# Optimization experiments

Hardware: AMD Instinct MI355X
Metric: run time of the kernel (lower is better)

Reference implementation:

```python
import jax, jax.numpy as jnp
import numpy as np

NUM_CAPSULE = 10
DIM_CAPSULE = 16
ROUTINGS = 3
EPS = 1e-7  # K.epsilon()


def squash(x, axis=-1):
    sq_norm = jnp.sum(jnp.square(x), axis=axis, keepdims=True) + EPS
    coeff = jnp.sqrt(sq_norm) / (1.0 + sq_norm)
    return coeff * x


def setup_inputs() -> dict:
    key = jax.random.key(0)
    k1, k2 = jax.random.split(key)
    B, I, Din = 64, 4096, 128
    u_vecs = jax.random.normal(k1, (B, I, Din), dtype=jnp.float32)
    # glorot-ish scale for the capsule kernel (flattened conv1d kernel of size 1)
    W = jax.random.normal(k2, (Din, NUM_CAPSULE * DIM_CAPSULE), dtype=jnp.float32) * 0.06
    return {"u_vecs": u_vecs, "W": W}


def reference(u_vecs, W):
    B, I, Din = u_vecs.shape
    N, D = NUM_CAPSULE, DIM_CAPSULE
    # conv1d with kernel size 1 == per-position matmul
    u_hat = jnp.einsum('bid,dk->bik', u_vecs, W)          # [B, I, N*D]
    u_hat = u_hat.reshape(B, I, N, D).transpose(0, 2, 1, 3)  # [B, N, I, D]

    b = jnp.zeros((B, N, I), dtype=u_hat.dtype)
    outputs = None
    for i in range(ROUTINGS):
        c = jax.nn.softmax(b, axis=1)                      # softmax over num_capsule
        s = jnp.einsum('bni,bnid->bnd', c, u_hat)          # weighted sum over input caps
        outputs = squash(s)                                # [B, N, D]
        if i < ROUTINGS - 1:
            b = jnp.einsum('bnd,bnid->bni', outputs, u_hat)  # agreement logits
    return outputs
```

## Files before the change

kernel.cpp:

```cpp
#include <hip/hip_runtime.h>
#include <hip/hip_bf16.h>
#include <math.h>

#define NCAP 10
#define DCAP 16
#define DIN  128
#define NPOS 4096
#define NB   64

typedef short short8 __attribute__((ext_vector_type(8)));
typedef float floatx4 __attribute__((ext_vector_type(4)));

__device__ inline float bflo(unsigned v) { return __uint_as_float(v << 16); }
__device__ inline float bfhi(unsigned v) { return __uint_as_float(v & 0xFFFF0000u); }
__device__ inline unsigned short f2bf(float f) {
    unsigned u = __float_as_uint(f);
    return (unsigned short)((u + 0x7FFFu + ((u >> 16) & 1u)) >> 16);
}
__device__ inline float bf2f(unsigned short h) { return __uint_as_float(((unsigned)h) << 16); }


__global__ __launch_bounds__(256) void gemm_uhat(const float* __restrict__ u,
                                                 const float* __restrict__ W,
                                                 uint4* __restrict__ uhat4,
                                                 float* __restrict__ partial) {
    const int b = blockIdx.x;
    const int blk = blockIdx.y;
    const int t = threadIdx.x;
    const int l = t & 63;
    const int wv = __builtin_amdgcn_readfirstlane(t >> 6);

    __shared__ __align__(16) char lds[62464];
    short* WT = (short*)lds;
    char* uio = lds + 40960;

    const float4* W4 = (const float4*)W;
    for (int i = t; i < 5120; i += 256) {
        const float4 wq = W4[i];
        const float* wqf = (const float*)&wq;
        const int k = i / 40;
        const int n0 = (i % 40) * 4;
        #pragma unroll
        for (int jj = 0; jj < 4; ++jj) {
            const int n = n0 + jj;
            WT[n * 128 + (((k >> 3) ^ (n & 15)) << 3) + (k & 7)] = f2bf(wqf[jj]);
        }
    }

    floatx4 cs0 = {0.f, 0.f, 0.f, 0.f}, cs1 = {0.f, 0.f, 0.f, 0.f};
    const float4* u4 = (const float4*)u;

    for (int cc = 0; cc < 4; ++cc) {
        __syncthreads();
        const int pos0 = blk * 256 + cc * 64;
        uint4* in4 = (uint4*)uio;

        #pragma unroll
        for (int i2 = 0; i2 < 4; ++i2) {
            const int q = t + i2 * 256;
            const int pos = q >> 4, ch = q & 15;
            const size_t g = ((size_t)b * NPOS + pos0 + pos) * 32 + ch * 2;
            const float4 x0 = u4[g];
            const float4 x1 = u4[g + 1];
            cs0.x += x0.x; cs0.y += x0.y; cs0.z += x0.z; cs0.w += x0.w;
            cs1.x += x1.x; cs1.y += x1.y; cs1.z += x1.z; cs1.w += x1.w;
            uint4 h;
            h.x = (unsigned)f2bf(x0.x) | ((unsigned)f2bf(x0.y) << 16);
            h.y = (unsigned)f2bf(x0.z) | ((unsigned)f2bf(x0.w) << 16);
            h.z = (unsigned)f2bf(x1.x) | ((unsigned)f2bf(x1.y) << 16);
            h.w = (unsigned)f2bf(x1.z) | ((unsigned)f2bf(x1.w) << 16);
            in4[pos * 16 + (ch ^ (pos & 15))] = h;
        }
        __syncthreads();

        const short8* in8 = (const short8*)uio;
        short8 af[4];
        #pragma unroll
        for (int kk = 0; kk < 4; ++kk)
            af[kk] = in8[(16 * wv + (l & 15)) * 16 + ((kk * 4 + (l >> 4)) ^ (l & 15))];

        floatx4 acc[10];
        const short8* wt8 = (const short8*)WT;
        #pragma unroll
        for (int n = 0; n < 10; ++n) {
            floatx4 a = {0.f, 0.f, 0.f, 0.f};
            #pragma unroll
            for (int kk = 0; kk < 4; ++kk) {
                const short8 bf = wt8[(n * 16 + (l & 15)) * 16 +
                                      ((kk * 4 + (l >> 4)) ^ (l & 15))];
                a = __builtin_amdgcn_mfma_f32_16x16x32_bf16(af[kk], bf, a, 0, 0, 0);
            }
            acc[n] = a;
        }
        __syncthreads();

        short* out16 = (short*)uio;
        #pragma unroll
        for (int n = 0; n < 10; ++n) {
            #pragma unroll
            for (int reg = 0; reg < 4; ++reg) {
                const int posl = 16 * wv + (l >> 4) * 4 + reg;
                out16[posl * 168 + n * 16 + (l & 15)] = f2bf(acc[n][reg]);
            }
        }
        __syncthreads();

        const uint4* o4 = (const uint4*)uio;
        #pragma unroll
        for (int i3 = 0; i3 < 5; ++i3) {
            const int q = t + i3 * 256;
            const int pos = q / 20, ch = q % 20;
            uhat4[((size_t)b * NPOS + pos0 + pos) * 20 + ch] = o4[pos * 21 + ch];
        }
    }

    #pragma unroll
    for (int mm = 16; mm <= 32; mm <<= 1) {
        cs0.x += __shfl_xor(cs0.x, mm); cs0.y += __shfl_xor(cs0.y, mm);
        cs0.z += __shfl_xor(cs0.z, mm); cs0.w += __shfl_xor(cs0.w, mm);
        cs1.x += __shfl_xor(cs1.x, mm); cs1.y += __shfl_xor(cs1.y, mm);
        cs1.z += __shfl_xor(cs1.z, mm); cs1.w += __shfl_xor(cs1.w, mm);
    }
    if (l < 16) {
        float4* p4 = (float4*)(partial + ((size_t)((b * 16 + blk) * 4 + wv)) * 128 + l * 8);
        p4[0] = make_float4(cs0.x, cs0.y, cs0.z, cs0.w);
        p4[1] = make_float4(cs1.x, cs1.y, cs1.z, cs1.w);
    }
}

__global__ __launch_bounds__(128) void small0(const float* __restrict__ partial,
                                              const float* __restrict__ W,
                                              float* __restrict__ vbuf) {
    const int b = blockIdx.x / NCAP;
    const int n = blockIdx.x % NCAP;
    const int t = threadIdx.x;
    __shared__ float xv[DIN];
    float a = 0.f;
    #pragma unroll 8
    for (int c = 0; c < 64; ++c)
        a += partial[(size_t)(b * 64 + c) * DIN + t];
    xv[t] = a;
    __syncthreads();
    if (t < DCAP) {
        float sv = 0.f;
        for (int d = 0; d < DIN; ++d)
            sv = fmaf(xv[d], W[d * 160 + n * DCAP + t], sv);
        sv *= 0.1f;
        float nq = sv * sv;
        #pragma unroll
        for (int mm = 8; mm >= 1; mm >>= 1) nq += __shfl_xor(nq, mm, 16);
        nq += 1e-7f;
        vbuf[(size_t)(b * NCAP + n) * DCAP + t] = sv * sqrtf(nq) / (1.0f + nq);
    }
}

__global__ __launch_bounds__(256, 4) void route_uhat(const uint4* __restrict__ uhat4,
                                                     const float* __restrict__ vbuf,
                                                     float* __restrict__ pws) {
    const int b = blockIdx.x;
    const int blk = blockIdx.y;
    const int t = threadIdx.x;
    const int l = t & 63;
    const int wv = __builtin_amdgcn_readfirstlane(t >> 6);

    __shared__ __align__(16) char tl[64 * 336];
    __shared__ float lgp[4][64][10];
    __shared__ float cs[64][10];
    short* tls = (short*)tl;
    uint4* tl4 = (uint4*)tl;

    const float* vb = vbuf + (size_t)b * 160;
    float acc = 0.f;

    for (int s = 0; s < 4; ++s) {
        __syncthreads();
        const size_t base4 = ((size_t)b * NPOS + blk * 256 + s * 64) * 20;
        #pragma unroll
        for (int i = 0; i < 5; ++i) {
            const int q = t + i * 256;
            tl4[(q / 20) * 21 + (q % 20)] = uhat4[base4 + q];
        }
        __syncthreads();

        float lg[10];
        #pragma unroll
        for (int n = 0; n < 10; ++n) {
            const uint2 uu = *(const uint2*)&tls[l * 168 + n * 16 + wv * 4];
            lg[n] = bflo(uu.x) * vb[n * 16 + wv * 4]
                  + bfhi(uu.x) * vb[n * 16 + wv * 4 + 1]
                  + bflo(uu.y) * vb[n * 16 + wv * 4 + 2]
                  + bfhi(uu.y) * vb[n * 16 + wv * 4 + 3];
            lgp[wv][l][n] = lg[n];
        }
        __syncthreads();

        float c[10];
        float m = -1e30f;
        #pragma unroll
        for (int n = 0; n < 10; ++n) {
            c[n] = lgp[0][l][n] + lgp[1][l][n] + lgp[2][l][n] + lgp[3][l][n];
            m = fmaxf(m, c[n]);
        }
        float ssum = 0.f;
        #pragma unroll
        for (int n = 0; n < 10; ++n) { c[n] = __expf(c[n] - m); ssum += c[n]; }
        const float inv = 1.0f / ssum;
        if (wv == 0) {
            #pragma unroll
            for (int n = 0; n < 10; ++n) cs[l][n] = c[n] * inv;
        }
        __syncthreads();

        if (t < 160) {
            const int n = t >> 4;
            for (int p = 0; p < 64; ++p)
                acc = fmaf(cs[p][n], bf2f((unsigned short)tls[p * 168 + t]), acc);
        }
    }
    if (t < 160) pws[(size_t)(b * 16 + blk) * 160 + t] = acc;
}

__global__ __launch_bounds__(256) void smallv(const float* __restrict__ pws,
                                              float* __restrict__ dst) {
    const int b = blockIdx.x;
    const int t = threadIdx.x;
    if (t >= 160) return;
    float a = 0.f;
    #pragma unroll
    for (int c = 0; c < 16; ++c)
        a += pws[(size_t)(b * 16 + c) * 160 + t];
    float nq = a * a;
    #pragma unroll
    for (int mm = 8; mm >= 1; mm >>= 1) nq += __shfl_xor(nq, mm, 16);
    nq += 1e-7f;
    dst[(size_t)b * 160 + t] = a * sqrtf(nq) / (1.0f + nq);
}


__global__ __launch_bounds__(256) void caps_sum(const float* __restrict__ u,
                                                float* __restrict__ partial) {
    const int b = blockIdx.x;
    const int chunk = blockIdx.y;
    const int t = threadIdx.x;
    const int v4 = t & 31;
    const int prow = t >> 5;
    const float4* up = (const float4*)u;
    const size_t posbase = (size_t)b * NPOS + chunk * 256;
    float4 acc = make_float4(0.f, 0.f, 0.f, 0.f);
    #pragma unroll 8
    for (int j = 0; j < 32; ++j) {
        float4 x = up[(posbase + prow + j * 8) * 32 + v4];
        acc.x += x.x; acc.y += x.y; acc.z += x.z; acc.w += x.w;
    }
    __shared__ float4 red[8][32];
    red[prow][v4] = acc;
    __syncthreads();
    if (t < 32) {
        float4 s = red[0][t];
        #pragma unroll
        for (int r = 1; r < 8; ++r) {
            s.x += red[r][t].x; s.y += red[r][t].y;
            s.z += red[r][t].z; s.w += red[r][t].w;
        }
        ((float4*)partial)[((size_t)b * 16 + chunk) * 32 + t] = s;
    }
}

template <int MODE>
__global__ __launch_bounds__(128) void caps_small(const float* __restrict__ src,
                                                  const float* __restrict__ W,
                                                  float* __restrict__ dst) {
    const int b = blockIdx.x / NCAP;
    const int n = blockIdx.x % NCAP;
    const int t = threadIdx.x;
    __shared__ float xv[DIN];
    __shared__ float vv[DCAP];
    float a = 0.f;
    if (MODE == 0) {
        #pragma unroll 4
        for (int c = 0; c < 16; ++c) a += src[(size_t)(b * 16 + c) * DIN + t];
    } else {
        #pragma unroll 4
        for (int c = 0; c < 16; ++c) a += src[((size_t)(b * 16 + c) * NCAP + n) * DIN + t];
    }
    xv[t] = a;
    __syncthreads();
    if (t < DCAP) {
        float sv = 0.f;
        for (int d = 0; d < DIN; ++d) sv = fmaf(xv[d], W[d * 160 + n * DCAP + t], sv);
        if (MODE == 0) sv *= 0.1f;
        float nq = sv * sv;
        #pragma unroll
        for (int mm = 8; mm >= 1; mm >>= 1) nq += __shfl_xor(nq, mm, 16);
        nq += 1e-7f;
        const float v = sv * sqrtf(nq) / (1.0f + nq);
        if (MODE == 2) dst[(size_t)(b * NCAP + n) * DCAP + t] = v;
        else vv[t] = v;
    }
    if (MODE != 2) {
        __syncthreads();
        float wd = 0.f;
        #pragma unroll
        for (int dd = 0; dd < DCAP; ++dd)
            wd = fmaf(W[t * 160 + n * DCAP + dd], vv[dd], wd);
        dst[(size_t)(b * NCAP + n) * DIN + t] = wd;
    }
}

__global__ __launch_bounds__(256, 3) void caps_route(const float* __restrict__ u,
                                                     const float* __restrict__ wsrc,
                                                     float* __restrict__ pdst) {
    const int b = blockIdx.x;
    const int tile = blockIdx.y;
    const int t = threadIdx.x;
    const int lane = t & 63;
    const int wv = __builtin_amdgcn_readfirstlane(t >> 6);
    __shared__ float4 tl4[64 * 32];
    __shared__ float lgp[4][64][11];
    float* tlf = (float*)tl4;
    const float4* wq4 = (const float4*)(wsrc + (size_t)b * (NCAP * DIN));
    float acc0[NCAP], acc1[NCAP];
    #pragma unroll
    for (int n = 0; n < NCAP; ++n) { acc0[n] = 0.f; acc1[n] = 0.f; }
    for (int s = 0; s < 4; ++s) {
        __syncthreads();
        const float4* src4 = (const float4*)u + ((size_t)b * NPOS + tile * 256 + s * 64) * 32;
        #pragma unroll
        for (int i = 0; i < 8; ++i) {
            const int q = t + i * 256;
            const int r = q >> 5, c = q & 31;
            tl4[r * 32 + (c ^ (r & 7))] = src4[q];
        }
        __syncthreads();
        float lg[NCAP];
        #pragma unroll
        for (int n = 0; n < NCAP; ++n) lg[n] = 0.f;
        #pragma unroll
        for (int j = 0; j < 8; ++j) {
            const float4 u4 = tl4[lane * 32 + wv * 8 + (j ^ (lane & 7))];
            #pragma unroll
            for (int n = 0; n < NCAP; ++n) {
                const float4 w4 = wq4[n * 32 + wv * 8 + j];
                lg[n] = fmaf(u4.x, w4.x, fmaf(u4.y, w4.y,
                        fmaf(u4.z, w4.z, fmaf(u4.w, w4.w, lg[n]))));
            }
        }
        #pragma unroll
        for (int n = 0; n < NCAP; ++n) lgp[wv][lane][n] = lg[n];
        __syncthreads();
        float c[NCAP];
        float m = -1e30f;
        #pragma unroll
        for (int n = 0; n < NCAP; ++n) {
            c[n] = lgp[0][lane][n] + lgp[1][lane][n] + lgp[2][lane][n] + lgp[3][lane][n];
            m = fmaxf(m, c[n]);
        }
        float ssum = 0.f;
        #pragma unroll
        for (int n = 0; n < NCAP; ++n) { c[n] = __expf(c[n] - m); ssum += c[n]; }
        const float inv = 1.0f / ssum;
        #pragma unroll
        for (int n = 0; n < NCAP; ++n) c[n] *= inv;
        const int col0 = lane >> 2, word = lane & 3;
        #pragma unroll
        for (int i = 0; i < 16; ++i) {
            const int p = wv * 16 + i;
            const int ca = col0 ^ (p & 7);
            const float u0 = tlf[(p * 32 + ca) * 4 + word];
            const float u1 = tlf[(p * 32 + ca + 16) * 4 + word];
            #pragma unroll
            for (int n = 0; n < NCAP; ++n) {
                const float cp = __int_as_float(
                    __builtin_amdgcn_readlane(__float_as_int(c[n]), p));
                acc0[n] = fmaf(cp, u0, acc0[n]);
                acc1[n] = fmaf(cp, u1, acc1[n]);
            }
        }
    }
    __syncthreads();
    float* red = tlf;
    #pragma unroll
    for (int n = 0; n < NCAP; ++n) {
        red[(wv * NCAP + n) * DIN + lane]      = acc0[n];
        red[(wv * NCAP + n) * DIN + lane + 64] = acc1[n];
    }
    __syncthreads();
    float* pb = pdst + (size_t)(b * 16 + tile) * (NCAP * DIN);
    for (int k = t; k < NCAP * DIN; k += 256)
        pb[k] = red[k] + red[1280 + k] + red[2560 + k] + red[3840 + k];
}

extern "C" void kernel_launch(void* const* d_in, const int* in_sizes, int n_in,
                              void* d_out, int out_size, void* d_ws, size_t ws_size,
                              hipStream_t stream) {
    const float* u = (const float*)d_in[0];
    const float* W = (const float*)d_in[1];
    float* out = (float*)d_out;
    char* wsb = (char*)d_ws;

    if (ws_size >= 86679552ull) {
        float* partial = (float*)wsb;
        float* vbuf    = (float*)(wsb + 2097152);
        float* pws     = (float*)(wsb + 2138112);
        uint4* uhat    = (uint4*)(wsb + 2793472);

        gemm_uhat<<<dim3(NB, 16), 256, 0, stream>>>(u, W, uhat, partial);
        small0<<<NB * NCAP, 128, 0, stream>>>(partial, W, vbuf);
        route_uhat<<<dim3(NB, 16), 256, 0, stream>>>(uhat, vbuf, pws);
        smallv<<<NB, 256, 0, stream>>>(pws, vbuf);
        route_uhat<<<dim3(NB, 16), 256, 0, stream>>>(uhat, vbuf, pws);
        smallv<<<NB, 256, 0, stream>>>(pws, out);
    } else {
        float* partial = (float*)wsb;
        float* wbuf    = (float*)wsb + 131072;
        float* pws32   = (float*)wsb + 212992;
        caps_sum<<<dim3(NB, 16), 256, 0, stream>>>(u, partial);
        caps_small<0><<<NB * NCAP, 128, 0, stream>>>(partial, W, wbuf);
        caps_route<<<dim3(NB, 16), 256, 0, stream>>>(u, wbuf, pws32);
        caps_small<1><<<NB * NCAP, 128, 0, stream>>>(pws32, W, wbuf);
        caps_route<<<dim3(NB, 16), 256, 0, stream>>>(u, wbuf, pws32);
        caps_small<2><<<NB * NCAP, 128, 0, stream>>>(pws32, W, out);
    }
}
```

Before: 106.8 us.

## Pre-swizzle W once in a prep kernel and load u directly into MFMA fragments

Adds a tiny wprep kernel that converts W to a swizzled bf16 layout once, so each gemm_uhat block copies it into LDS instead of re-transposing and converting W itself. The GEMM now reads u straight from global memory into MFMA A fragments, skipping the LDS staging pass and two barriers per tile. The output is staged through a smaller LDS region in two halves, which cuts LDS use and allows an occupancy hint of 3 blocks per CU. Column sums are reduced per block, so the partial buffer is four times smaller and small0 reads fewer entries. The cost is an extra kernel launch and less coalesced u loads, since each lane fetches 32-byte pieces of separate rows.

```diff
diff --git a/kernel.cpp b/kernel.cpp
--- a/kernel.cpp
+++ b/kernel.cpp
@@ -20,67 +20,70 @@
 __device__ inline float bf2f(unsigned short h) { return __uint_as_float(((unsigned)h) << 16); }
 
 
-__global__ __launch_bounds__(256) void gemm_uhat(const float* __restrict__ u,
-                                                 const float* __restrict__ W,
-                                                 uint4* __restrict__ uhat4,
-                                                 float* __restrict__ partial) {
+__global__ __launch_bounds__(256) void wprep(const float* __restrict__ W,
+                                             uint4* __restrict__ WTg) {
+    const int cid = blockIdx.x * 256 + threadIdx.x;
+    if (cid >= 2560) return;
+    const int row = cid >> 4;
+    const int csn = cid & 15;
+    const int kc = csn ^ (row & 15);
+    unsigned p[4];
+    #pragma unroll
+    for (int e = 0; e < 4; ++e) {
+        const float a = W[(kc * 8 + e * 2) * 160 + row];
+        const float b = W[(kc * 8 + e * 2 + 1) * 160 + row];
+        p[e] = (unsigned)f2bf(a) | ((unsigned)f2bf(b) << 16);
+    }
+    WTg[cid] = make_uint4(p[0], p[1], p[2], p[3]);
+}
+
+__global__ __launch_bounds__(256, 3) void gemm_uhat(const float* __restrict__ u,
+                                                    const uint4* __restrict__ WTg,
+                                                    uint4* __restrict__ uhat4,
+                                                    float* __restrict__ partial) {
     const int b = blockIdx.x;
     const int blk = blockIdx.y;
     const int t = threadIdx.x;
     const int l = t & 63;
     const int wv = __builtin_amdgcn_readfirstlane(t >> 6);
 
-    __shared__ __align__(16) char lds[62464];
-    short* WT = (short*)lds;
-    char* uio = lds + 40960;
-
-    const float4* W4 = (const float4*)W;
-    for (int i = t; i < 5120; i += 256) {
-        const float4 wq = W4[i];
-        const float* wqf = (const float*)&wq;
-        const int k = i / 40;
-        const int n0 = (i % 40) * 4;
-        #pragma unroll
-        for (int jj = 0; jj < 4; ++jj) {
-            const int n = n0 + jj;
-            WT[n * 128 + (((k >> 3) ^ (n & 15)) << 3) + (k & 7)] = f2bf(wqf[jj]);
-        }
-    }
-
-    floatx4 cs0 = {0.f, 0.f, 0.f, 0.f}, cs1 = {0.f, 0.f, 0.f, 0.f};
-    const float4* u4 = (const float4*)u;
-
-    for (int cc = 0; cc < 4; ++cc) {
-        __syncthreads();
-        const int pos0 = blk * 256 + cc * 64;
-        uint4* in4 = (uint4*)uio;
-
-        #pragma unroll
-        for (int i2 = 0; i2 < 4; ++i2) {
-            const int q = t + i2 * 256;
-            const int pos = q >> 4, ch = q & 15;
-            const size_t g = ((size_t)b * NPOS + pos0 + pos) * 32 + ch * 2;
-            const float4 x0 = u4[g];
-            const float4 x1 = u4[g + 1];
-            cs0.x += x0.x; cs0.y += x0.y; cs0.z += x0.z; cs0.w += x0.w;
-            cs1.x += x1.x; cs1.y += x1.y; cs1.z += x1.z; cs1.w += x1.w;
-            uint4 h;
-            h.x = (unsigned)f2bf(x0.x) | ((unsigned)f2bf(x0.y) << 16);
-            h.y = (unsigned)f2bf(x0.z) | ((unsigned)f2bf(x0.w) << 16);
-            h.z = (unsigned)f2bf(x1.x) | ((unsigned)f2bf(x1.y) << 16);
-            h.w = (unsigned)f2bf(x1.z) | ((unsigned)f2bf(x1.w) << 16);
-            in4[pos * 16 + (ch ^ (pos & 15))] = h;
-        }
-        __syncthreads();
-
-        const short8* in8 = (const short8*)uio;
+    __shared__ __align__(16) char lds[40960 + 11264];
+    uint4* WT4 = (uint4*)lds;
+    short* out16 = (short*)(lds + 40960);
+    float* csbuf = (float*)(lds + 40960);
+
+    #pragma unroll
+    for (int i = 0; i < 10; ++i)
+        WT4[t + i * 256] = WTg[t + i * 256];
+    __syncthreads();
+
+    float cs[4][8];
+    #pragma unroll
+    for (int kk = 0; kk < 4; ++kk)
+        #pragma unroll
+        for (int e = 0; e < 8; ++e) cs[kk][e] = 0.f;
+
+    const short8* wt8 = (const short8*)lds;
+    const float4* u4g = (const float4*)u;
+
+    for (int mt = 0; mt < 4; ++mt) {
+        const size_t row = (size_t)b * NPOS + blk * 256 + mt * 64 + wv * 16 + (l & 15);
         short8 af[4];
         #pragma unroll
-        for (int kk = 0; kk < 4; ++kk)
-            af[kk] = in8[(16 * wv + (l & 15)) * 16 + ((kk * 4 + (l >> 4)) ^ (l & 15))];
+        for (int kk = 0; kk < 4; ++kk) {
+            const float4 x0 = u4g[row * 32 + kk * 8 + (l >> 4) * 2];
+            const float4 x1 = u4g[row * 32 + kk * 8 + (l >> 4) * 2 + 1];
+            cs[kk][0] += x0.x; cs[kk][1] += x0.y; cs[kk][2] += x0.z; cs[kk][3] += x0.w;
+            cs[kk][4] += x1.x; cs[kk][5] += x1.y; cs[kk][6] += x1.z; cs[kk][7] += x1.w;
+            short8 a;
+            a[0] = (short)f2bf(x0.x); a[1] = (short)f2bf(x0.y);
+            a[2] = (short)f2bf(x0.z); a[3] = (short)f2bf(x0.w);
+            a[4] = (short)f2bf(x1.x); a[5] = (short)f2bf(x1.y);
+            a[6] = (short)f2bf(x1.z); a[7] = (short)f2bf(x1.w);
+            af[kk] = a;
+        }
 
         floatx4 acc[10];
-        const short8* wt8 = (const short8*)WT;
         #pragma unroll
         for (int n = 0; n < 10; ++n) {
             floatx4 a = {0.f, 0.f, 0.f, 0.f};
@@ -92,40 +95,52 @@
             }
             acc[n] = a;
         }
-        __syncthreads();
-
-        short* out16 = (short*)uio;
-        #pragma unroll
-        for (int n = 0; n < 10; ++n) {
-            #pragma unroll
-            for (int reg = 0; reg < 4; ++reg) {
-                const int posl = 16 * wv + (l >> 4) * 4 + reg;
-                out16[posl * 168 + n * 16 + (l & 15)] = f2bf(acc[n][reg]);
+
+        #pragma unroll
+        for (int h = 0; h < 2; ++h) {
+            __syncthreads();
+            if ((wv >> 1) == h) {
+                const int r0 = (wv & 1) * 16 + (l >> 4) * 4;
+                #pragma unroll
+                for (int n = 0; n < 10; ++n)
+                    #pragma unroll
+                    for (int reg = 0; reg < 4; ++reg)
+                        out16[(r0 + reg) * 176 + n * 16 + (l & 15)] =
+                            (short)f2bf(acc[n][reg]);
             }
-        }
-        __syncthreads();
-
-        const uint4* o4 = (const uint4*)uio;
-        #pragma unroll
-        for (int i3 = 0; i3 < 5; ++i3) {
-            const int q = t + i3 * 256;
-            const int pos = q / 20, ch = q % 20;
-            uhat4[((size_t)b * NPOS + pos0 + pos) * 20 + ch] = o4[pos * 21 + ch];
-        }
-    }
-
-    #pragma unroll
-    for (int mm = 16; mm <= 32; mm <<= 1) {
-        cs0.x += __shfl_xor(cs0.x, mm); cs0.y += __shfl_xor(cs0.y, mm);
-        cs0.z += __shfl_xor(cs0.z, mm); cs0.w += __shfl_xor(cs0.w, mm);
-        cs1.x += __shfl_xor(cs1.x, mm); cs1.y += __shfl_xor(cs1.y, mm);
-        cs1.z += __shfl_xor(cs1.z, mm); cs1.w += __shfl_xor(cs1.w, mm);
-    }
-    if (l < 16) {
-        float4* p4 = (float4*)(partial + ((size_t)((b * 16 + blk) * 4 + wv)) * 128 + l * 8);
-        p4[0] = make_float4(cs0.x, cs0.y, cs0.z, cs0.w);
-        p4[1] = make_float4(cs1.x, cs1.y, cs1.z, cs1.w);
-    }
+            __syncthreads();
+            const uint4* o4 = (const uint4*)out16;
+            const size_t gb = ((size_t)b * NPOS + blk * 256 + mt * 64 + h * 32) * 20;
+            #pragma unroll
+            for (int i = 0; i < 3; ++i) {
+                const int q = t + i * 256;
+                if (q < 640)
+                    uhat4[gb + q] = o4[(q / 20) * 22 + (q % 20)];
+            }
+        }
+    }
+
+    __syncthreads();
+    #pragma unroll
+    for (int kk = 0; kk < 4; ++kk)
+        #pragma unroll
+        for (int e = 0; e < 8; ++e) {
+            float v = cs[kk][e];
+            v += __shfl_xor(v, 1); v += __shfl_xor(v, 2);
+            v += __shfl_xor(v, 4); v += __shfl_xor(v, 8);
+            cs[kk][e] = v;
+        }
+    if ((l & 15) == 0) {
+        #pragma unroll
+        for (int kk = 0; kk < 4; ++kk)
+            #pragma unroll
+            for (int e = 0; e < 8; ++e)
+                csbuf[wv * 128 + kk * 32 + (l >> 4) * 8 + e] = cs[kk][e];
+    }
+    __syncthreads();
+    if (t < 128)
+        partial[(size_t)(b * 16 + blk) * 128 + t] =
+            csbuf[t] + csbuf[128 + t] + csbuf[256 + t] + csbuf[384 + t];
 }
 
 __global__ __launch_bounds__(128) void small0(const float* __restrict__ partial,
@@ -136,9 +151,9 @@
     const int t = threadIdx.x;
     __shared__ float xv[DIN];
     float a = 0.f;
-    #pragma unroll 8
-    for (int c = 0; c < 64; ++c)
-        a += partial[(size_t)(b * 64 + c) * DIN + t];
+    #pragma unroll 4
+    for (int c = 0; c < 16; ++c)
+        a += partial[(size_t)(b * 16 + c) * DIN + t];
     xv[t] = a;
     __syncthreads();
     if (t < DCAP) {
@@ -398,13 +413,15 @@
     float* out = (float*)d_out;
     char* wsb = (char*)d_ws;
 
-    if (ws_size >= 86679552ull) {
+    if (ws_size >= 85147648ull) {
         float* partial = (float*)wsb;
-        float* vbuf    = (float*)(wsb + 2097152);
-        float* pws     = (float*)(wsb + 2138112);
-        uint4* uhat    = (uint4*)(wsb + 2793472);
-
-        gemm_uhat<<<dim3(NB, 16), 256, 0, stream>>>(u, W, uhat, partial);
+        float* vbuf    = (float*)(wsb + 524288);
+        float* pws     = (float*)(wsb + 565248);
+        uint4* WTg     = (uint4*)(wsb + 1220608);
+        uint4* uhat    = (uint4*)(wsb + 1261568);
+
+        wprep<<<10, 256, 0, stream>>>(W, WTg);
+        gemm_uhat<<<dim3(NB, 16), 256, 0, stream>>>(u, WTg, uhat, partial);
         small0<<<NB * NCAP, 128, 0, stream>>>(partial, W, vbuf);
         route_uhat<<<dim3(NB, 16), 256, 0, stream>>>(uhat, vbuf, pws);
         smallv<<<NB, 256, 0, stream>>>(pws, vbuf);
```

Result: slower. 111.2 us (+4.2%).
